# Performance work log

Hardware: AMD Instinct MI355X
Metric: run time of the kernel (lower is better)

The kernel has to match this reference:

```python
import jax, jax.numpy as jnp
import numpy as np

N = 35          # nodes (hardcoded by x.repeat(35,1,1))
V = 4           # edge views
D1, D2, D3 = 512, 256, 128


def _full_graph_edges():
    # fully connected, no self loops, COO [2, E], E = 35*34
    src, dst = np.meshgrid(np.arange(N), np.arange(N), indexing='ij')
    mask = src != dst
    return np.stack([src[mask], dst[mask]], axis=0).astype(np.int64)


def setup_inputs() -> dict:
    key = jax.random.key(0)
    ks = jax.random.split(key, 8)
    E = N * (N - 1)
    edge_index = jnp.asarray(_full_graph_edges())
    s1, s2, s3 = 1.0 / np.sqrt(V), 1.0 / np.sqrt(V), 1.0 / np.sqrt(V)
    return {
        'x': jnp.ones((N, 1), jnp.float32),
        'edge_attr': jax.random.uniform(ks[0], (E, V), jnp.float32),
        'edge_index': edge_index,
        'mlp1_w': jax.random.normal(ks[1], (V, 1 * D1), jnp.float32) * s1,
        'mlp1_b': jnp.zeros((1 * D1,), jnp.float32),
        'root1': jax.random.normal(ks[2], (1, D1), jnp.float32),
        'bias1': jnp.zeros((D1,), jnp.float32),
        'mlp2_w': jax.random.normal(ks[3], (V, D1 * D2), jnp.float32) * s2,
        'mlp2_b': jnp.zeros((D1 * D2,), jnp.float32),
        'root2': jax.random.normal(ks[4], (D1, D2), jnp.float32) / np.sqrt(D1),
        'bias2': jnp.zeros((D2,), jnp.float32),
        'mlp3_w': jax.random.normal(ks[5], (V, D2 * D3), jnp.float32) * s3,
        'mlp3_b': jnp.zeros((D2 * D3,), jnp.float32),
        'root3': jax.random.normal(ks[6], (D2, D3), jnp.float32) / np.sqrt(D2),
        'bias3': jnp.zeros((D3,), jnp.float32),
    }


def _nnconv(x, edge_attr, src, dst, mlp_w, mlp_b, root, bias, in_c, out_c):
    # edge MLP -> per-edge weight matrix [E, in_c, out_c]
    w = jax.nn.relu(edge_attr @ mlp_w + mlp_b).reshape(-1, in_c, out_c)
    # gather source feats, per-edge matmul: [E, out_c]
    msg = jnp.einsum('ei,eio->eo', x[src], w)
    # scatter-mean to targets
    agg = jax.ops.segment_sum(msg, dst, num_segments=N)
    cnt = jax.ops.segment_sum(jnp.ones_like(msg[:, 0]), dst, num_segments=N)
    agg = agg / jnp.maximum(cnt, 1.0)[:, None]
    return agg + x @ root + bias


def reference(x, edge_attr, edge_index, mlp1_w, mlp1_b, root1, bias1,
              mlp2_w, mlp2_b, root2, bias2, mlp3_w, mlp3_b, root3, bias3):
    src, dst = edge_index[0], edge_index[1]
    h = jax.nn.relu(_nnconv(x, edge_attr, src, dst, mlp1_w, mlp1_b, root1, bias1, 1, D1))
    h = jax.nn.relu(_nnconv(h, edge_attr, src, dst, mlp2_w, mlp2_b, root2, bias2, D1, D2))
    h = jax.nn.relu(_nnconv(h, edge_attr, src, dst, mlp3_w, mlp3_b, root3, bias3, D2, D3))
    # cbt[a, i] = sum_f |h[i, f] - h[a, f]|   (repeat / transpose / abs / sum)
    cbt = jnp.sum(jnp.abs(h[None, :, :] - h[:, None, :]), axis=2)
    return cbt
```

## Files before the change

kernel.cpp:

```cpp
#include <hip/hip_runtime.h>

#define NN 35

typedef float v2f __attribute__((ext_vector_type(2)));

__device__ __forceinline__ v2f pk_fma(v2f a, v2f b, v2f c) {
#if __has_builtin(__builtin_elementwise_fma)
    return __builtin_elementwise_fma(a, b, c);
#else
    v2f d; d.x = fmaf(a.x, b.x, c.x); d.y = fmaf(a.y, b.y, c.y); return d;
#endif
}
__device__ __forceinline__ v2f pk_relu(v2f a) {
    v2f d; d.x = fmaxf(a.x, 0.f); d.y = fmaxf(a.y, 0.f); return d;
}
__device__ __forceinline__ v2f pk_splat(float s) { v2f d; d.x = s; d.y = s; return d; }
__device__ __forceinline__ v2f pk_make(float a, float b) { v2f d; d.x = a; d.y = b; return d; }

__device__ __forceinline__ float agld(const float* p) {
    return __hip_atomic_load(p, __ATOMIC_RELAXED, __HIP_MEMORY_SCOPE_AGENT);
}


__global__ __launch_bounds__(512)
void layer1_kernel(const float* __restrict__ x,
                   const float* __restrict__ ea,
                   const float* __restrict__ W1, const float* __restrict__ b1,
                   const float* __restrict__ root1, const float* __restrict__ bias1,
                   float* __restrict__ h1,
                   float* __restrict__ aggz)
{
    const int d = blockIdx.x;
    const int o = threadIdx.x;
    const int gtid = d * 512 + o;
    if (gtid < 35 * 384) aggz[gtid] = 0.f;
    if (gtid == 35 * 384) ((unsigned*)aggz)[13440] = 0u;

    const float w0 = W1[o], w1 = W1[512 + o], w2 = W1[1024 + o], w3 = W1[1536 + o];
    const float bb = b1[o];
    float sum = 0.f;
#pragma unroll
    for (int s = 0; s < NN; ++s) {
        if (s == d) continue;
        const float4 a = ((const float4*)ea)[s * 34 + (d < s ? d : d - 1)];
        float w = fmaf(a.x, w0, fmaf(a.y, w1, fmaf(a.z, w2, fmaf(a.w, w3, bb))));
        sum = fmaf(x[s], fmaxf(w, 0.f), sum);
    }
    h1[gtid] = fmaxf(sum * (1.f / 34.f) + x[d] * root1[o] + bias1[o], 0.f);
}

__global__ __launch_bounds__(256, 2)
void edge2_kernel(const float* __restrict__ h,
                  const float* __restrict__ ea,
                  const float* __restrict__ W,
                  const float* __restrict__ bias,
                  const float* __restrict__ root,
                  float* __restrict__ agg)
{
    const int d  = blockIdx.x;
    const int c  = blockIdx.y;
    const int i0 = c * 16;
    const int o  = threadIdx.x;

    __shared__ __align__(16) float hs[35][16];
    __shared__ float4 as[34];

    if (o < 35) {
        const int s = (o < 34) ? (o + (o >= d ? 1 : 0)) : d;
        const float4* hp = (const float4*)(h + (size_t)s * 512 + i0);
#pragma unroll
        for (int k = 0; k < 4; ++k) ((float4*)hs[o])[k] = hp[k];
    }
    if (o >= 64 && o < 98) {
        const int j = o - 64;
        const int s = j + (j >= d ? 1 : 0);
        as[j] = ((const float4*)ea)[s * 34 + (d < s ? d : d - 1)];
    }
    __syncthreads();

    v2f Wv0[8], Wv1[8], Wv2[8], Wv3[8], BB[8], RR[8];
#pragma unroll
    for (int p = 0; p < 8; ++p) {
        const size_t b0 = (size_t)(i0 + 2 * p) * 256 + o;
        const size_t bq = b0 + 256;
        Wv0[p] = pk_make(W[b0],          W[bq]);
        Wv1[p] = pk_make(W[131072 + b0], W[131072 + bq]);
        Wv2[p] = pk_make(W[262144 + b0], W[262144 + bq]);
        Wv3[p] = pk_make(W[393216 + b0], W[393216 + bq]);
        BB[p]  = pk_make(bias[b0],       bias[bq]);
        RR[p]  = pk_make(root[b0],       root[bq]);
    }

    v2f acc0 = pk_splat(0.f), acc1 = pk_splat(0.f);
#pragma unroll 2
    for (int j = 0; j < 34; ++j) {
        const float4 a = as[j];
        const v2f ax = pk_splat(a.x), ay = pk_splat(a.y);
        const v2f az = pk_splat(a.z), aw = pk_splat(a.w);
#pragma unroll
        for (int k = 0; k < 4; ++k) {
            const float4 hv = ((const float4*)hs[j])[k];
            {
                const int p = k * 2;
                v2f w = pk_fma(ax, Wv0[p], pk_fma(ay, Wv1[p],
                        pk_fma(az, Wv2[p], pk_fma(aw, Wv3[p], BB[p]))));
                acc0 = pk_fma(pk_make(hv.x, hv.y), pk_relu(w), acc0);
            }
            {
                const int p = k * 2 + 1;
                v2f w = pk_fma(ax, Wv0[p], pk_fma(ay, Wv1[p],
                        pk_fma(az, Wv2[p], pk_fma(aw, Wv3[p], BB[p]))));
                acc1 = pk_fma(pk_make(hv.z, hv.w), pk_relu(w), acc1);
            }
        }
    }
    v2f racc = pk_splat(0.f);
#pragma unroll
    for (int k = 0; k < 4; ++k) {
        const float4 hv = ((const float4*)hs[34])[k];
        racc = pk_fma(pk_make(hv.x, hv.y), RR[k * 2],     racc);
        racc = pk_fma(pk_make(hv.z, hv.w), RR[k * 2 + 1], racc);
    }
    const float acc = acc0.x + acc0.y + acc1.x + acc1.y;
    atomicAdd(&agg[d * 256 + o], acc * (1.f / 34.f) + (racc.x + racc.y));
}

__global__ __launch_bounds__(128, 2)
void edge3cbt_kernel(const float* __restrict__ agg2,
                     const float* __restrict__ bias2,
                     const float* __restrict__ ea,
                     const float* __restrict__ W,
                     const float* __restrict__ bias,
                     const float* __restrict__ root,
                     const float* __restrict__ bias3,
                     float* __restrict__ agg,
                     unsigned* __restrict__ cnt,
                     float* __restrict__ out)
{
    const int d  = blockIdx.x;
    const int c  = blockIdx.y;
    const int i0 = c * 8;
    const int o  = threadIdx.x;

    __shared__ __align__(16) float hs[35][8];
    __shared__ float4 as[34];
    __shared__ unsigned ticket_s;

    if (o < 70) {
        const int r = o >> 1, k = o & 1;
        const int s = (r < 34) ? (r + (r >= d ? 1 : 0)) : d;
        float4 v = ((const float4*)(agg2 + (size_t)s * 256 + i0))[k];
        const float4 bv = ((const float4*)(bias2 + i0))[k];
        v.x = fmaxf(v.x + bv.x, 0.f);
        v.y = fmaxf(v.y + bv.y, 0.f);
        v.z = fmaxf(v.z + bv.z, 0.f);
        v.w = fmaxf(v.w + bv.w, 0.f);
        ((float4*)hs[r])[k] = v;
    }
    if (o >= 94) {
        const int j = o - 94;
        const int s = j + (j >= d ? 1 : 0);
        as[j] = ((const float4*)ea)[s * 34 + (d < s ? d : d - 1)];
    }
    __syncthreads();

    v2f Wv0[4], Wv1[4], Wv2[4], Wv3[4], BB[4], RR[4];
#pragma unroll
    for (int p = 0; p < 4; ++p) {
        const size_t b0 = (size_t)(i0 + 2 * p) * 128 + o;
        const size_t bq = b0 + 128;
        Wv0[p] = pk_make(W[b0],         W[bq]);
        Wv1[p] = pk_make(W[32768 + b0], W[32768 + bq]);
        Wv2[p] = pk_make(W[65536 + b0], W[65536 + bq]);
        Wv3[p] = pk_make(W[98304 + b0], W[98304 + bq]);
        BB[p]  = pk_make(bias[b0],      bias[bq]);
        RR[p]  = pk_make(root[b0],      root[bq]);
    }

    v2f acc0 = pk_splat(0.f), acc1 = pk_splat(0.f);
#pragma unroll 2
    for (int j = 0; j < 34; ++j) {
        const float4 a = as[j];
        const v2f ax = pk_splat(a.x), ay = pk_splat(a.y);
        const v2f az = pk_splat(a.z), aw = pk_splat(a.w);
#pragma unroll
        for (int k = 0; k < 2; ++k) {
            const float4 hv = ((const float4*)hs[j])[k];
            {
                const int p = k * 2;
                v2f w = pk_fma(ax, Wv0[p], pk_fma(ay, Wv1[p],
                        pk_fma(az, Wv2[p], pk_fma(aw, Wv3[p], BB[p]))));
                acc0 = pk_fma(pk_make(hv.x, hv.y), pk_relu(w), acc0);
            }
            {
                const int p = k * 2 + 1;
                v2f w = pk_fma(ax, Wv0[p], pk_fma(ay, Wv1[p],
                        pk_fma(az, Wv2[p], pk_fma(aw, Wv3[p], BB[p]))));
                acc1 = pk_fma(pk_make(hv.z, hv.w), pk_relu(w), acc1);
            }
        }
    }
    v2f racc = pk_splat(0.f);
#pragma unroll
    for (int k = 0; k < 2; ++k) {
        const float4 hv = ((const float4*)hs[34])[k];
        racc = pk_fma(pk_make(hv.x, hv.y), RR[k * 2],     racc);
        racc = pk_fma(pk_make(hv.z, hv.w), RR[k * 2 + 1], racc);
    }
    const float acc = acc0.x + acc0.y + acc1.x + acc1.y;
    atomicAdd(&agg[d * 128 + o], acc * (1.f / 34.f) + (racc.x + racc.y));

    __syncthreads();
    if (o == 0) {
        __threadfence();
        ticket_s = atomicAdd(cnt, 1u);
    }
    __syncthreads();
    const int slot = (int)ticket_s - (NN * 32 - NN);
    if (slot < 0) return;

    if (o == 0) {
        while (__hip_atomic_load(cnt, __ATOMIC_ACQUIRE, __HIP_MEMORY_SCOPE_AGENT)
               < (unsigned)(NN * 32))
            __builtin_amdgcn_s_sleep(1);
    }
    __syncthreads();
    __threadfence();

    const int a_ = slot;
    const int lane = o & 63, w = o >> 6;
    const float b0 = bias3[lane], b1 = bias3[64 + lane];
    const float va0 = fmaxf(agld(&agg[a_ * 128 + lane])      + b0, 0.f);
    const float va1 = fmaxf(agld(&agg[a_ * 128 + 64 + lane]) + b1, 0.f);
    for (int i = w; i < NN; i += 2) {
        const float vi0 = fmaxf(agld(&agg[i * 128 + lane])      + b0, 0.f);
        const float vi1 = fmaxf(agld(&agg[i * 128 + 64 + lane]) + b1, 0.f);
        float s = fabsf(vi0 - va0) + fabsf(vi1 - va1);
#pragma unroll
        for (int off = 32; off > 0; off >>= 1)
            s += __shfl_xor(s, off, 64);
        if (lane == 0) out[a_ * NN + i] = s;
    }
}

extern "C" void kernel_launch(void* const* d_in, const int* in_sizes, int n_in,
                              void* d_out, int out_size, void* d_ws, size_t ws_size,
                              hipStream_t stream) {
    const float* x      = (const float*)d_in[0];
    const float* ea     = (const float*)d_in[1];
    const float* mlp1_w = (const float*)d_in[3];
    const float* mlp1_b = (const float*)d_in[4];
    const float* root1  = (const float*)d_in[5];
    const float* bias1  = (const float*)d_in[6];
    const float* mlp2_w = (const float*)d_in[7];
    const float* mlp2_b = (const float*)d_in[8];
    const float* root2  = (const float*)d_in[9];
    const float* bias2  = (const float*)d_in[10];
    const float* mlp3_w = (const float*)d_in[11];
    const float* mlp3_b = (const float*)d_in[12];
    const float* root3  = (const float*)d_in[13];
    const float* bias3  = (const float*)d_in[14];
    float* out = (float*)d_out;

    float* ws   = (float*)d_ws;
    float* agg2 = ws;
    float* agg3 = ws + 8960;
    unsigned* cnt = (unsigned*)(ws + 13440);
    float* h1   = ws + 13444;

    layer1_kernel<<<NN, 512, 0, stream>>>(x, ea, mlp1_w, mlp1_b, root1, bias1, h1, ws);
    edge2_kernel<<<dim3(NN, 32), 256, 0, stream>>>(h1, ea, mlp2_w, mlp2_b, root2, agg2);
    edge3cbt_kernel<<<dim3(NN, 32), 128, 0, stream>>>(agg2, bias2, ea, mlp3_w, mlp3_b,
                                                      root3, bias3, agg3, cnt, out);
}
```

Measured before the change: 157.0 us.

## Split edge kernels finer and move pairwise L1 distance into separate kernel

Layer-2 blocks now cover 8 input channels instead of 16, doubling the grid to 35x64 with half the per-thread register weights. Layer-3 blocks use 256 threads, with two thread groups each handling 4 input channels, so fewer registers are needed per thread. The atomic-ticket grid sync and fused distance tail are replaced by a standalone cbt kernel launched afterward. The aim is more parallelism and no spin-wait serialization, at the cost of an extra launch and more atomics on the aggregation buffers.

```diff
diff --git a/kernel.cpp b/kernel.cpp
--- a/kernel.cpp
+++ b/kernel.cpp
@@ -16,10 +16,6 @@
 }
 __device__ __forceinline__ v2f pk_splat(float s) { v2f d; d.x = s; d.y = s; return d; }
 __device__ __forceinline__ v2f pk_make(float a, float b) { v2f d; d.x = a; d.y = b; return d; }
-
-__device__ __forceinline__ float agld(const float* p) {
-    return __hip_atomic_load(p, __ATOMIC_RELAXED, __HIP_MEMORY_SCOPE_AGENT);
-}
 
 
 __global__ __launch_bounds__(512)
@@ -34,7 +30,6 @@
     const int o = threadIdx.x;
     const int gtid = d * 512 + o;
     if (gtid < 35 * 384) aggz[gtid] = 0.f;
-    if (gtid == 35 * 384) ((unsigned*)aggz)[13440] = 0u;
 
     const float w0 = W1[o], w1 = W1[512 + o], w2 = W1[1024 + o], w3 = W1[1536 + o];
     const float bb = b1[o];
@@ -59,28 +54,15 @@
 {
     const int d  = blockIdx.x;
     const int c  = blockIdx.y;
-    const int i0 = c * 16;
+    const int i0 = c * 8;
     const int o  = threadIdx.x;
 
-    __shared__ __align__(16) float hs[35][16];
+    __shared__ __align__(16) float hs[35][8];
     __shared__ float4 as[34];
 
-    if (o < 35) {
-        const int s = (o < 34) ? (o + (o >= d ? 1 : 0)) : d;
-        const float4* hp = (const float4*)(h + (size_t)s * 512 + i0);
-#pragma unroll
-        for (int k = 0; k < 4; ++k) ((float4*)hs[o])[k] = hp[k];
-    }
-    if (o >= 64 && o < 98) {
-        const int j = o - 64;
-        const int s = j + (j >= d ? 1 : 0);
-        as[j] = ((const float4*)ea)[s * 34 + (d < s ? d : d - 1)];
-    }
-    __syncthreads();
-
-    v2f Wv0[8], Wv1[8], Wv2[8], Wv3[8], BB[8], RR[8];
-#pragma unroll
-    for (int p = 0; p < 8; ++p) {
+    v2f Wv0[4], Wv1[4], Wv2[4], Wv3[4], BB[4], RR[4];
+#pragma unroll
+    for (int p = 0; p < 4; ++p) {
         const size_t b0 = (size_t)(i0 + 2 * p) * 256 + o;
         const size_t bq = b0 + 256;
         Wv0[p] = pk_make(W[b0],          W[bq]);
@@ -91,91 +73,17 @@
         RR[p]  = pk_make(root[b0],       root[bq]);
     }
 
-    v2f acc0 = pk_splat(0.f), acc1 = pk_splat(0.f);
-#pragma unroll 2
-    for (int j = 0; j < 34; ++j) {
-        const float4 a = as[j];
-        const v2f ax = pk_splat(a.x), ay = pk_splat(a.y);
-        const v2f az = pk_splat(a.z), aw = pk_splat(a.w);
-#pragma unroll
-        for (int k = 0; k < 4; ++k) {
-            const float4 hv = ((const float4*)hs[j])[k];
-            {
-                const int p = k * 2;
-                v2f w = pk_fma(ax, Wv0[p], pk_fma(ay, Wv1[p],
-                        pk_fma(az, Wv2[p], pk_fma(aw, Wv3[p], BB[p]))));
-                acc0 = pk_fma(pk_make(hv.x, hv.y), pk_relu(w), acc0);
-            }
-            {
-                const int p = k * 2 + 1;
-                v2f w = pk_fma(ax, Wv0[p], pk_fma(ay, Wv1[p],
-                        pk_fma(az, Wv2[p], pk_fma(aw, Wv3[p], BB[p]))));
-                acc1 = pk_fma(pk_make(hv.z, hv.w), pk_relu(w), acc1);
-            }
-        }
-    }
-    v2f racc = pk_splat(0.f);
-#pragma unroll
-    for (int k = 0; k < 4; ++k) {
-        const float4 hv = ((const float4*)hs[34])[k];
-        racc = pk_fma(pk_make(hv.x, hv.y), RR[k * 2],     racc);
-        racc = pk_fma(pk_make(hv.z, hv.w), RR[k * 2 + 1], racc);
-    }
-    const float acc = acc0.x + acc0.y + acc1.x + acc1.y;
-    atomicAdd(&agg[d * 256 + o], acc * (1.f / 34.f) + (racc.x + racc.y));
-}
-
-__global__ __launch_bounds__(128, 2)
-void edge3cbt_kernel(const float* __restrict__ agg2,
-                     const float* __restrict__ bias2,
-                     const float* __restrict__ ea,
-                     const float* __restrict__ W,
-                     const float* __restrict__ bias,
-                     const float* __restrict__ root,
-                     const float* __restrict__ bias3,
-                     float* __restrict__ agg,
-                     unsigned* __restrict__ cnt,
-                     float* __restrict__ out)
-{
-    const int d  = blockIdx.x;
-    const int c  = blockIdx.y;
-    const int i0 = c * 8;
-    const int o  = threadIdx.x;
-
-    __shared__ __align__(16) float hs[35][8];
-    __shared__ float4 as[34];
-    __shared__ unsigned ticket_s;
-
     if (o < 70) {
         const int r = o >> 1, k = o & 1;
         const int s = (r < 34) ? (r + (r >= d ? 1 : 0)) : d;
-        float4 v = ((const float4*)(agg2 + (size_t)s * 256 + i0))[k];
-        const float4 bv = ((const float4*)(bias2 + i0))[k];
-        v.x = fmaxf(v.x + bv.x, 0.f);
-        v.y = fmaxf(v.y + bv.y, 0.f);
-        v.z = fmaxf(v.z + bv.z, 0.f);
-        v.w = fmaxf(v.w + bv.w, 0.f);
-        ((float4*)hs[r])[k] = v;
-    }
-    if (o >= 94) {
-        const int j = o - 94;
+        ((float4*)hs[r])[k] = ((const float4*)(h + (size_t)s * 512 + i0))[k];
+    }
+    if (o >= 70 && o < 104) {
+        const int j = o - 70;
         const int s = j + (j >= d ? 1 : 0);
         as[j] = ((const float4*)ea)[s * 34 + (d < s ? d : d - 1)];
     }
     __syncthreads();
-
-    v2f Wv0[4], Wv1[4], Wv2[4], Wv3[4], BB[4], RR[4];
-#pragma unroll
-    for (int p = 0; p < 4; ++p) {
-        const size_t b0 = (size_t)(i0 + 2 * p) * 128 + o;
-        const size_t bq = b0 + 128;
-        Wv0[p] = pk_make(W[b0],         W[bq]);
-        Wv1[p] = pk_make(W[32768 + b0], W[32768 + bq]);
-        Wv2[p] = pk_make(W[65536 + b0], W[65536 + bq]);
-        Wv3[p] = pk_make(W[98304 + b0], W[98304 + bq]);
-        BB[p]  = pk_make(bias[b0],      bias[bq]);
-        RR[p]  = pk_make(root[b0],      root[bq]);
-    }
 
     v2f acc0 = pk_splat(0.f), acc1 = pk_splat(0.f);
 #pragma unroll 2
@@ -208,39 +116,109 @@
         racc = pk_fma(pk_make(hv.z, hv.w), RR[k * 2 + 1], racc);
     }
     const float acc = acc0.x + acc0.y + acc1.x + acc1.y;
+    atomicAdd(&agg[d * 256 + o], acc * (1.f / 34.f) + (racc.x + racc.y));
+}
+
+__global__ __launch_bounds__(256, 2)
+void edge3_kernel(const float* __restrict__ agg2,
+                  const float* __restrict__ bias2,
+                  const float* __restrict__ ea,
+                  const float* __restrict__ W,
+                  const float* __restrict__ bias,
+                  const float* __restrict__ root,
+                  float* __restrict__ agg)
+{
+    const int d   = blockIdx.x;
+    const int c   = blockIdx.y;
+    const int i0  = c * 8;
+    const int thr = threadIdx.x;
+    const int o   = thr & 127;
+    const int g   = thr >> 7;
+
+    __shared__ __align__(16) float hs[35][8];
+    __shared__ float4 as[34];
+
+    v2f Wv0[2], Wv1[2], Wv2[2], Wv3[2], BB[2], RR[2];
+#pragma unroll
+    for (int p = 0; p < 2; ++p) {
+        const size_t b0 = (size_t)(i0 + g * 4 + 2 * p) * 128 + o;
+        const size_t bq = b0 + 128;
+        Wv0[p] = pk_make(W[b0],         W[bq]);
+        Wv1[p] = pk_make(W[32768 + b0], W[32768 + bq]);
+        Wv2[p] = pk_make(W[65536 + b0], W[65536 + bq]);
+        Wv3[p] = pk_make(W[98304 + b0], W[98304 + bq]);
+        BB[p]  = pk_make(bias[b0],      bias[bq]);
+        RR[p]  = pk_make(root[b0],      root[bq]);
+    }
+
+    if (thr < 70) {
+        const int r = thr >> 1, k = thr & 1;
+        const int s = (r < 34) ? (r + (r >= d ? 1 : 0)) : d;
+        float4 v = ((const float4*)(agg2 + (size_t)s * 256 + i0))[k];
+        const float4 bv = ((const float4*)(bias2 + i0))[k];
+        v.x = fmaxf(v.x + bv.x, 0.f);
+        v.y = fmaxf(v.y + bv.y, 0.f);
+        v.z = fmaxf(v.z + bv.z, 0.f);
+        v.w = fmaxf(v.w + bv.w, 0.f);
+        ((float4*)hs[r])[k] = v;
+    }
+    if (thr >= 70 && thr < 104) {
+        const int j = thr - 70;
+        const int s = j + (j >= d ? 1 : 0);
+        as[j] = ((const float4*)ea)[s * 34 + (d < s ? d : d - 1)];
+    }
+    __syncthreads();
+
+    v2f acc0 = pk_splat(0.f), acc1 = pk_splat(0.f);
+#pragma unroll 2
+    for (int j = 0; j < 34; ++j) {
+        const float4 a = as[j];
+        const v2f ax = pk_splat(a.x), ay = pk_splat(a.y);
+        const v2f az = pk_splat(a.z), aw = pk_splat(a.w);
+        const float4 hv = ((const float4*)hs[j])[g];
+        {
+            v2f w = pk_fma(ax, Wv0[0], pk_fma(ay, Wv1[0],
+                    pk_fma(az, Wv2[0], pk_fma(aw, Wv3[0], BB[0]))));
+            acc0 = pk_fma(pk_make(hv.x, hv.y), pk_relu(w), acc0);
+        }
+        {
+            v2f w = pk_fma(ax, Wv0[1], pk_fma(ay, Wv1[1],
+                    pk_fma(az, Wv2[1], pk_fma(aw, Wv3[1], BB[1]))));
+            acc1 = pk_fma(pk_make(hv.z, hv.w), pk_relu(w), acc1);
+        }
+    }
+    v2f racc = pk_splat(0.f);
+    {
+        const float4 hv = ((const float4*)hs[34])[g];
+        racc = pk_fma(pk_make(hv.x, hv.y), RR[0], racc);
+        racc = pk_fma(pk_make(hv.z, hv.w), RR[1], racc);
+    }
+    const float acc = acc0.x + acc0.y + acc1.x + acc1.y;
     atomicAdd(&agg[d * 128 + o], acc * (1.f / 34.f) + (racc.x + racc.y));
-
-    __syncthreads();
-    if (o == 0) {
-        __threadfence();
-        ticket_s = atomicAdd(cnt, 1u);
-    }
-    __syncthreads();
-    const int slot = (int)ticket_s - (NN * 32 - NN);
-    if (slot < 0) return;
-
-    if (o == 0) {
-        while (__hip_atomic_load(cnt, __ATOMIC_ACQUIRE, __HIP_MEMORY_SCOPE_AGENT)
-               < (unsigned)(NN * 32))
-            __builtin_amdgcn_s_sleep(1);
-    }
-    __syncthreads();
-    __threadfence();
-
-    const int a_ = slot;
-    const int lane = o & 63, w = o >> 6;
-    const float b0 = bias3[lane], b1 = bias3[64 + lane];
-    const float va0 = fmaxf(agld(&agg[a_ * 128 + lane])      + b0, 0.f);
-    const float va1 = fmaxf(agld(&agg[a_ * 128 + 64 + lane]) + b1, 0.f);
-    for (int i = w; i < NN; i += 2) {
-        const float vi0 = fmaxf(agld(&agg[i * 128 + lane])      + b0, 0.f);
-        const float vi1 = fmaxf(agld(&agg[i * 128 + 64 + lane]) + b1, 0.f);
-        float s = fabsf(vi0 - va0) + fabsf(vi1 - va1);
-#pragma unroll
-        for (int off = 32; off > 0; off >>= 1)
-            s += __shfl_xor(s, off, 64);
-        if (lane == 0) out[a_ * NN + i] = s;
-    }
+}
+
+__global__ __launch_bounds__(256)
+void cbt_kernel(const float* __restrict__ agg3,
+                const float* __restrict__ bias3,
+                float* __restrict__ out)
+{
+    const int wv = blockIdx.x * 4 + (threadIdx.x >> 6);
+    const int lane = threadIdx.x & 63;
+    if (wv >= NN * NN) return;
+    const int a_ = wv / NN, i_ = wv % NN;
+    float s = 0.f;
+#pragma unroll
+    for (int q = 0; q < 2; ++q) {
+        const int f = lane + q * 64;
+        const float bb = bias3[f];
+        const float hi = fmaxf(agg3[i_ * 128 + f] + bb, 0.f);
+        const float ha = fmaxf(agg3[a_ * 128 + f] + bb, 0.f);
+        s += fabsf(hi - ha);
+    }
+#pragma unroll
+    for (int off = 32; off > 0; off >>= 1)
+        s += __shfl_xor(s, off, 64);
+    if (lane == 0) out[wv] = s;
 }
 
 extern "C" void kernel_launch(void* const* d_in, const int* in_sizes, int n_in,
@@ -264,12 +242,11 @@
 
     float* ws   = (float*)d_ws;
     float* agg2 = ws;
-    float* agg3 = ws + 8960;
-    unsigned* cnt = (unsigned*)(ws + 13440);
-    float* h1   = ws + 13444;
-
-    layer1_kernel<<<NN, 512, 0, stream>>>(x, ea, mlp1_w, mlp1_b, root1, bias1, h1, ws);
-    edge2_kernel<<<dim3(NN, 32), 256, 0, stream>>>(h1, ea, mlp2_w, mlp2_b, root2, agg2);
-    edge3cbt_kernel<<<dim3(NN, 32), 128, 0, stream>>>(agg2, bias2, ea, mlp3_w, mlp3_b,
-                                                      root3, bias3, agg3, cnt, out);
-}
+    float* agg3 = agg2 + 35 * 256;
+    float* h1   = agg3 + 35 * 128;
+
+    layer1_kernel<<<NN, 512, 0, stream>>>(x, ea, mlp1_w, mlp1_b, root1, bias1, h1, agg2);
+    edge2_kernel<<<dim3(NN, 64), 256, 0, stream>>>(h1, ea, mlp2_w, mlp2_b, root2, agg2);
+    edge3_kernel<<<dim3(NN, 32), 256, 0, stream>>>(agg2, bias2, ea, mlp3_w, mlp3_b, root3, agg3);
+    cbt_kernel<<<(NN * NN + 3) / 4, 256, 0, stream>>>(agg3, bias3, out);
+}
```

New measurement: 128.4 us, median of 2. 1.22x faster.
